# Performance work log

Hardware: AMD Instinct MI355X
Metric: run time of the kernel (lower is better)

Reference implementation:

```python
import jax, jax.numpy as jnp
import numpy as np

WINDOW_SIZE = 11
SIGMA = 1.5
CHANNELS = 3
PAD = WINDOW_SIZE // 2


def make_window():
    xs = np.arange(WINDOW_SIZE)
    g = np.exp(-((xs - WINDOW_SIZE // 2) ** 2) / (2.0 * SIGMA ** 2))
    g = g / g.sum()
    w2d = np.outer(g, g).astype(np.float32)  # [11,11]
    # depthwise kernel in OIHW with groups=3: [3,1,11,11]
    return jnp.asarray(np.broadcast_to(w2d, (CHANNELS, 1, WINDOW_SIZE, WINDOW_SIZE)).copy())


def setup_inputs() -> dict:
    key = jax.random.key(0)
    k1, k2 = jax.random.split(key)
    x = jax.random.uniform(k1, (16, 3, 512, 512), dtype=jnp.float32)
    y = jax.random.uniform(k2, (16, 3, 512, 512), dtype=jnp.float32)
    window = make_window()
    return {"x": x, "y": y, "window": window}


def _dwconv(img, window):
    # depthwise 2D conv, padding=5, groups=3 (NCHW / OIHW)
    return jax.lax.conv_general_dilated(
        img, window,
        window_strides=(1, 1),
        padding=[(PAD, PAD), (PAD, PAD)],
        feature_group_count=CHANNELS,
        dimension_numbers=("NCHW", "OIHW", "NCHW"),
    )


def reference(x, y, window):
    mu1 = _dwconv(x, window)
    mu2 = _dwconv(y, window)
    mu1_sq = mu1 * mu1
    mu2_sq = mu2 * mu2
    mu1_mu2 = mu1 * mu2
    sigma1_sq = _dwconv(x * x, window) - mu1_sq
    sigma2_sq = _dwconv(y * y, window) - mu2_sq
    sigma12 = _dwconv(x * y, window) - mu1_mu2
    c1 = 0.01 ** 2
    c2 = 0.03 ** 2
    ssim = ((2.0 * mu1_mu2 + c1) * (2.0 * sigma12 + c2)) / (
        (mu1_sq + mu2_sq + c1) * (sigma1_sq + sigma2_sq + c2))
    return jnp.mean(ssim)
```

## Files before the change

kernel.cpp:

```cpp
#include <hip/hip_runtime.h>


#define IMG_H 512
#define IMG_W 512
#define NC    48

constexpr int TW = 64;
constexpr int TH = 16;
constexpr int SW = 78;
constexpr int SH = 26;
constexpr int SS = 78;
constexpr int VW = 76;
constexpr int NBLK = (IMG_W / TW) * (IMG_H / TH) * NC;

__global__ __launch_bounds__(256, 4)
void ssim_fused(const float* __restrict__ x, const float* __restrict__ y,
                const float* __restrict__ w, double* __restrict__ part,
                int use_atomic)
{
    __shared__ __align__(16) float sx[SH][SS];
    __shared__ __align__(16) float sy[SH][SS];
    __shared__ __align__(16) float vv[5][TH][VW];
    __shared__ float wsum[4];

    const int tid = threadIdx.x;
    const int x0 = blockIdx.x * TW - 8;
    const int y0 = blockIdx.y * TH - 5;
    const float* __restrict__ xp = x + (size_t)blockIdx.z * (IMG_H * IMG_W);
    const float* __restrict__ yp = y + (size_t)blockIdx.z * (IMG_H * IMG_W);

    float g[11];
    {
        const float g5inv = 1.0f / sqrtf(w[55 + 5]);
        #pragma unroll
        for (int k = 0; k < 11; ++k) g[k] = w[55 + k] * g5inv;
    }

    for (int i = tid; i < SH * SW; i += 256) {
        const int r = i / SW;
        const int c = i - r * SW;
        const int gr = y0 + r, gc = x0 + c;
        const bool ok = (gr >= 0) & (gr < IMG_H) & (gc >= 0) & (gc < IMG_W);
        const size_t idx = (size_t)gr * IMG_W + gc;
        sx[r][c] = ok ? xp[idx] : 0.0f;
        sy[r][c] = ok ? yp[idx] : 0.0f;
    }
    __syncthreads();

    for (int t = tid; t < 75 * 4; t += 256) {
        const int c  = t % 75;
        const int r0 = (t / 75) << 2;
        float xv[14], yv[14], xxv[14], yyv[14], xyv[14];
        #pragma unroll
        for (int k = 0; k < 14; ++k) {
            const float a = sx[r0 + k][c + 2];
            const float b = sy[r0 + k][c + 2];
            xv[k] = a; yv[k] = b;
            xxv[k] = a * a; yyv[k] = b * b; xyv[k] = a * b;
        }
        #pragma unroll
        for (int j = 0; j < 4; ++j) {
            float s0 = 0.f, s1 = 0.f, s2 = 0.f, s3 = 0.f, s4 = 0.f;
            #pragma unroll
            for (int k = 0; k < 11; ++k) {
                const float gk = g[k];
                s0 = fmaf(gk, xv[j + k],  s0);
                s1 = fmaf(gk, yv[j + k],  s1);
                s2 = fmaf(gk, xxv[j + k], s2);
                s3 = fmaf(gk, yyv[j + k], s3);
                s4 = fmaf(gk, xyv[j + k], s4);
            }
            vv[0][r0 + j][c] = s0;
            vv[1][r0 + j][c] = s1;
            vv[2][r0 + j][c] = s2;
            vv[3][r0 + j][c] = s3;
            vv[4][r0 + j][c] = s4;
        }
    }
    __syncthreads();

    const int r  = tid >> 4;
    const int j0 = (tid & 15) << 2;

    float acc[5][4];
    #pragma unroll
    for (int q = 0; q < 5; ++q) {
        const float4* vp = (const float4*)(&vv[q][r][j0]);
        const float4 A = vp[0], B = vp[1], C = vp[2], D = vp[3];
        const float win[16] = {A.x, A.y, A.z, A.w, B.x, B.y, B.z, B.w,
                               C.x, C.y, C.z, C.w, D.x, D.y, D.z, D.w};
        #pragma unroll
        for (int t = 0; t < 4; ++t) {
            float s = 0.f;
            #pragma unroll
            for (int k = 0; k < 11; ++k) s = fmaf(g[k], win[t + 1 + k], s);
            acc[q][t] = s;
        }
    }

    const float C1 = 1e-4f;
    const float C2 = 9e-4f;
    float local = 0.0f;
    #pragma unroll
    for (int t = 0; t < 4; ++t) {
        const float m1 = acc[0][t], m2 = acc[1][t];
        const float m1s = m1 * m1, m2s = m2 * m2, m12 = m1 * m2;
        const float v1  = acc[2][t] - m1s;
        const float v2  = acc[3][t] - m2s;
        const float v12 = acc[4][t] - m12;
        const float num = (2.0f * m12 + C1) * (2.0f * v12 + C2);
        const float den = (m1s + m2s + C1) * (v1 + v2 + C2);
        local += num / den;
    }

    #pragma unroll
    for (int off = 32; off > 0; off >>= 1)
        local += __shfl_down(local, off, 64);
    if ((tid & 63) == 0) wsum[tid >> 6] = local;
    __syncthreads();
    if (tid == 0) {
        const double blk = (double)wsum[0] + (double)wsum[1]
                         + (double)wsum[2] + (double)wsum[3];
        if (use_atomic) {
            atomicAdd(part, blk);
        } else {
            const int bflat = blockIdx.x
                            + gridDim.x * (blockIdx.y + gridDim.y * blockIdx.z);
            part[bflat] = blk;
        }
    }
}

__global__ void ssim_reduce(const double* __restrict__ part, float* __restrict__ out,
                            int n)
{
    __shared__ double s[256];
    double t = 0.0;
    for (int i = threadIdx.x; i < n; i += 256) t += part[i];
    s[threadIdx.x] = t;
    __syncthreads();
    for (int off = 128; off > 0; off >>= 1) {
        if (threadIdx.x < off) s[threadIdx.x] += s[threadIdx.x + off];
        __syncthreads();
    }
    if (threadIdx.x == 0)
        out[0] = (float)(s[0] / (double)((size_t)NC * IMG_H * IMG_W));
}

extern "C" void kernel_launch(void* const* d_in, const int* in_sizes, int n_in,
                              void* d_out, int out_size, void* d_ws, size_t ws_size,
                              hipStream_t stream)
{
    const float* x = (const float*)d_in[0];
    const float* y = (const float*)d_in[1];
    const float* w = (const float*)d_in[2];
    double* part = (double*)d_ws;

    const bool fits = ws_size >= (size_t)NBLK * sizeof(double);
    dim3 grid(IMG_W / TW, IMG_H / TH, NC);

    if (fits) {
        ssim_fused<<<grid, 256, 0, stream>>>(x, y, w, part, 0);
        ssim_reduce<<<1, 256, 0, stream>>>(part, (float*)d_out, NBLK);
    } else {
        hipMemsetAsync(d_ws, 0, sizeof(double), stream);
        ssim_fused<<<grid, 256, 0, stream>>>(x, y, w, part, 1);
        ssim_reduce<<<1, 256, 0, stream>>>(part, (float*)d_out, 1);
    }
}
```

Measured before the change: 225.7 us.

## Load input tile directly from global memory into registers, drop shared staging

Removes the shared-memory staging of the x/y tile and its barrier. The vertical-pass threads now read their 14-row column strips straight from global memory, with a fast unguarded path for interior blocks and a clamped, masked path at borders. It also forces the Gaussian weights into scalar registers via readfirstlane and raises the occupancy hint to 6 waves. Overlapping strips from neighbouring threads now each re-read global memory (relying on cache) instead of sharing one LDS copy, and register pressure under the tighter launch bound may rise.

```diff
diff --git a/kernel.cpp b/kernel.cpp
--- a/kernel.cpp
+++ b/kernel.cpp
@@ -7,19 +7,14 @@
 
 constexpr int TW = 64;
 constexpr int TH = 16;
-constexpr int SW = 78;
-constexpr int SH = 26;
-constexpr int SS = 78;
 constexpr int VW = 76;
 constexpr int NBLK = (IMG_W / TW) * (IMG_H / TH) * NC;
 
-__global__ __launch_bounds__(256, 4)
+__global__ __launch_bounds__(256, 6)
 void ssim_fused(const float* __restrict__ x, const float* __restrict__ y,
                 const float* __restrict__ w, double* __restrict__ part,
                 int use_atomic)
 {
-    __shared__ __align__(16) float sx[SH][SS];
-    __shared__ __align__(16) float sy[SH][SS];
     __shared__ __align__(16) float vv[5][TH][VW];
     __shared__ float wsum[4];
 
@@ -33,30 +28,44 @@
     {
         const float g5inv = 1.0f / sqrtf(w[55 + 5]);
         #pragma unroll
-        for (int k = 0; k < 11; ++k) g[k] = w[55 + k] * g5inv;
+        for (int k = 0; k < 11; ++k)
+            g[k] = __uint_as_float(
+                (unsigned)__builtin_amdgcn_readfirstlane(
+                    (int)__float_as_uint(w[55 + k] * g5inv)));
     }
 
-    for (int i = tid; i < SH * SW; i += 256) {
-        const int r = i / SW;
-        const int c = i - r * SW;
-        const int gr = y0 + r, gc = x0 + c;
-        const bool ok = (gr >= 0) & (gr < IMG_H) & (gc >= 0) & (gc < IMG_W);
-        const size_t idx = (size_t)gr * IMG_W + gc;
-        sx[r][c] = ok ? xp[idx] : 0.0f;
-        sy[r][c] = ok ? yp[idx] : 0.0f;
-    }
-    __syncthreads();
+    const bool interior = (y0 >= 0) & (y0 + 25 < IMG_H)
+                        & (x0 + 2 >= 0) & (x0 + 76 < IMG_W);
 
     for (int t = tid; t < 75 * 4; t += 256) {
-        const int c  = t % 75;
-        const int r0 = (t / 75) << 2;
+        const int c   = t % 75;
+        const int r0  = (t / 75) << 2;
+        const int gc  = x0 + c + 2;
+        const int gr0 = y0 + r0;
         float xv[14], yv[14], xxv[14], yyv[14], xyv[14];
-        #pragma unroll
-        for (int k = 0; k < 14; ++k) {
-            const float a = sx[r0 + k][c + 2];
-            const float b = sy[r0 + k][c + 2];
-            xv[k] = a; yv[k] = b;
-            xxv[k] = a * a; yyv[k] = b * b; xyv[k] = a * b;
+        if (interior) {
+            const unsigned base = (unsigned)(gr0 * IMG_W + gc);
+            #pragma unroll
+            for (int k = 0; k < 14; ++k) {
+                const float a = xp[base + (unsigned)(k * IMG_W)];
+                const float b = yp[base + (unsigned)(k * IMG_W)];
+                xv[k] = a; yv[k] = b;
+                xxv[k] = a * a; yyv[k] = b * b; xyv[k] = a * b;
+            }
+        } else {
+            const int  cc  = min(max(gc, 0), IMG_W - 1);
+            const bool okc = ((unsigned)gc < (unsigned)IMG_W);
+            #pragma unroll
+            for (int k = 0; k < 14; ++k) {
+                const int  gr = gr0 + k;
+                const int  cr = min(max(gr, 0), IMG_H - 1);
+                const bool ok = okc & ((unsigned)gr < (unsigned)IMG_H);
+                const unsigned idx = (unsigned)(cr * IMG_W + cc);
+                const float a = ok ? xp[idx] : 0.0f;
+                const float b = ok ? yp[idx] : 0.0f;
+                xv[k] = a; yv[k] = b;
+                xxv[k] = a * a; yyv[k] = b * b; xyv[k] = a * b;
+            }
         }
         #pragma unroll
         for (int j = 0; j < 4; ++j) {
```

Measured after the change: 184.2 us. -18.4%, faster.
